# Kernel optimization log

Measured on AMD Instinct MI355X. Metric: run time of the kernel, lower is better.

The kernel has to match this reference:

```python
import jax, jax.numpy as jnp
import numpy as np

N_NODES = 10000
DEG = 32            # max_edges (fixed degree after padding)
CHANNELS = 16
IN_DIM = 4
BATCH = 8


def setup_inputs() -> dict:
    key = jax.random.key(0)
    k1, k2, k3 = jax.random.split(key, 3)
    E = N_NODES * DEG
    x = jax.random.normal(k1, (BATCH, N_NODES, IN_DIM), dtype=jnp.float32)
    # neighbor indices in [0, N_NODES]; index N_NODES is the padded 'useless' zero node
    edges = jax.random.randint(k2, (E,), 0, N_NODES + 1, dtype=jnp.int64)
    # torch.rand init: uniform [0,1); one weight tensor per input channel
    weights = jax.random.uniform(k3, (IN_DIM, E, CHANNELS), dtype=jnp.float32)
    return {"x": x, "edges": edges, "weights": weights}


def reference(x, edges, weights):
    B, N, in_dim = x.shape
    E = edges.shape[0]
    deg = E // N
    C = weights.shape[-1]
    # append zero 'useless node' so padding index N gathers zeros
    x_pad = jnp.concatenate([x, jnp.zeros((B, 1, in_dim), dtype=x.dtype)], axis=1)  # [B, N+1, in_dim]
    # super_edges = cat([edges]*C); viewed as [E, C] row-major (matches torch .view)
    idx = jnp.tile(edges, C).reshape(E, C)  # [E, C]
    out = jnp.zeros((B, N, C), dtype=x.dtype)
    for i in range(in_dim):  # small fixed loop over input channels (distinct weights)
        g = x_pad[:, :, i]              # [B, N+1]
        toc = g[:, idx]                 # gather -> [B, E, C]
        conv = toc * weights[i]         # per-edge weights broadcast over batch
        out = out + conv.reshape(B, N, deg, C).sum(axis=2)  # fixed-window segment sum
    return out
```

## Files before the change

### kernel.cpp

```cpp
#include <hip/hip_runtime.h>
#include <hip/hip_bf16.h>

#define N_NODES 10000
#define DEG     32
#define CH      16
#define IN_DIM  4
#define BATCH   8
#define E_EDGES (N_NODES * DEG)
#define WI_STRIDE (E_EDGES * CH)
#define P_COUNT 625
#define LX_STRIDE 36

__global__ __launch_bounds__(256) void lcg_transpose(const float* __restrict__ x,
                                                     float* __restrict__ xt) {
    int t = blockIdx.x * 256 + threadIdx.x;
    if (t < BATCH * N_NODES) {
        int b = t / N_NODES;
        int node = t - b * N_NODES;
        float4 v = *(const float4*)(x + 4 * t);
        *(float4*)(xt + node * 32 + b * 4) = v;
    } else if (t < BATCH * N_NODES + 8) {
        int r = t - BATCH * N_NODES;
        *(float4*)(xt + N_NODES * 32 + r * 4) = make_float4(0.f, 0.f, 0.f, 0.f);
    }
}

__global__ __launch_bounds__(1024, 8) void lcg_main(
    const float* __restrict__ xt,
    const int*   __restrict__ edges,
    const float* __restrict__ w,
    float*       __restrict__ out)
{
    __shared__ float lx[512 * LX_STRIDE];

    int p = blockIdx.x;
    int t = threadIdx.x;

    {
        int sub = t & 7;
        int rg  = t >> 3;
        const int* ep = edges + 512 * p;
        int nd[4];
#pragma unroll
        for (int k = 0; k < 4; k++) nd[k] = ep[rg + 128 * k];
#pragma unroll
        for (int k = 0; k < 4; k++) {
            int s = rg + 128 * k;
            float4 v = *(const float4*)(xt + nd[k] * 32 + sub * 4);
            *(float4*)(&lx[s * LX_STRIDE + sub * 4]) = v;
        }
    }
    __syncthreads();

    int lane = t & 63;
    int j    = t >> 6;
    int c    = lane & 15;
    int dq   = lane >> 4;
    int n    = p + P_COUNT * j;

    const float* wb = w + n * (DEG * CH) + lane;

    float acc[BATCH];
#pragma unroll
    for (int b = 0; b < BATCH; b++) acc[b] = 0.0f;

    const float* lrow = &lx[(16 * dq + c) * LX_STRIDE];

#pragma unroll 1
    for (int ds = 0; ds < 8; ds++) {
        float w0 = wb[64 * ds];
        float w1 = wb[64 * ds + WI_STRIDE];
        float w2 = wb[64 * ds + 2 * WI_STRIDE];
        float w3 = wb[64 * ds + 3 * WI_STRIDE];
        const float* lr = lrow + ds * (64 * LX_STRIDE);
#pragma unroll
        for (int b = 0; b < BATCH; b++) {
            float4 xq = *(const float4*)(lr + 4 * b);
            acc[b] += xq.x * w0 + xq.y * w1 + xq.z * w2 + xq.w * w3;
        }
    }

#pragma unroll
    for (int b = 0; b < BATCH; b++) {
        acc[b] += __shfl_xor(acc[b], 16, 64);
        acc[b] += __shfl_xor(acc[b], 32, 64);
    }

    int ob = n * CH + c;
    out[(2 * dq + 0) * (N_NODES * CH) + ob] = acc[2 * dq + 0];
    out[(2 * dq + 1) * (N_NODES * CH) + ob] = acc[2 * dq + 1];
}

extern "C" void kernel_launch(void* const* d_in, const int* in_sizes, int n_in,
                              void* d_out, int out_size, void* d_ws, size_t ws_size,
                              hipStream_t stream) {
    const float* x     = (const float*)d_in[0];
    const int*   edges = (const int*)d_in[1];
    const float* w     = (const float*)d_in[2];
    float* out = (float*)d_out;
    float* xt  = (float*)d_ws;

    int tr_total  = BATCH * N_NODES + 8;
    int tr_blocks = (tr_total + 255) / 256;
    lcg_transpose<<<tr_blocks, 256, 0, stream>>>(x, xt);

    lcg_main<<<P_COUNT, 1024, 0, stream>>>(xt, edges, w, out);
}
```

Baseline: 130.5 us.

## Drop transpose kernel, gather x directly, and software-prefetch weights

Removes the separate transpose launch and has the main kernel gather x straight from its original [B,N,4] layout, substituting zeros for the padding node. It also loads the first weights before the shared-memory fill and prefetches the next step's weights inside the loop, so global-load latency overlaps with compute. This saves one kernel launch and a pass over x. In exchange, each gather now reads scattered 16-byte chunks per batch instead of contiguous 128-byte rows, and the wrapped prefetch on the last iteration issues redundant loads.

```diff
diff --git a/kernel.cpp b/kernel.cpp
--- a/kernel.cpp
+++ b/kernel.cpp
@@ -1,5 +1,4 @@
 #include <hip/hip_runtime.h>
-#include <hip/hip_bf16.h>
 
 #define N_NODES 10000
 #define DEG     32
@@ -11,22 +10,8 @@
 #define P_COUNT 625
 #define LX_STRIDE 36
 
-__global__ __launch_bounds__(256) void lcg_transpose(const float* __restrict__ x,
-                                                     float* __restrict__ xt) {
-    int t = blockIdx.x * 256 + threadIdx.x;
-    if (t < BATCH * N_NODES) {
-        int b = t / N_NODES;
-        int node = t - b * N_NODES;
-        float4 v = *(const float4*)(x + 4 * t);
-        *(float4*)(xt + node * 32 + b * 4) = v;
-    } else if (t < BATCH * N_NODES + 8) {
-        int r = t - BATCH * N_NODES;
-        *(float4*)(xt + N_NODES * 32 + r * 4) = make_float4(0.f, 0.f, 0.f, 0.f);
-    }
-}
-
 __global__ __launch_bounds__(1024, 8) void lcg_main(
-    const float* __restrict__ xt,
+    const float* __restrict__ x,
     const int*   __restrict__ edges,
     const float* __restrict__ w,
     float*       __restrict__ out)
@@ -36,9 +21,22 @@
     int p = blockIdx.x;
     int t = threadIdx.x;
 
+    int lane = t & 63;
+    int j    = t >> 6;
+    int c    = lane & 15;
+    int dq   = lane >> 4;
+    int n    = p + P_COUNT * j;
+
+    const float* wb = w + n * (DEG * CH) + lane;
+
+    float w0 = wb[0];
+    float w1 = wb[WI_STRIDE];
+    float w2 = wb[2 * WI_STRIDE];
+    float w3 = wb[3 * WI_STRIDE];
+
     {
-        int sub = t & 7;
-        int rg  = t >> 3;
+        int b  = t & 7;
+        int rg = t >> 3;
         const int* ep = edges + 512 * p;
         int nd[4];
 #pragma unroll
@@ -46,19 +44,13 @@
 #pragma unroll
         for (int k = 0; k < 4; k++) {
             int s = rg + 128 * k;
-            float4 v = *(const float4*)(xt + nd[k] * 32 + sub * 4);
-            *(float4*)(&lx[s * LX_STRIDE + sub * 4]) = v;
+            float4 v = make_float4(0.f, 0.f, 0.f, 0.f);
+            if (nd[k] < N_NODES)
+                v = *(const float4*)(x + (b * N_NODES + nd[k]) * 4);
+            *(float4*)(&lx[s * LX_STRIDE + b * 4]) = v;
         }
     }
     __syncthreads();
-
-    int lane = t & 63;
-    int j    = t >> 6;
-    int c    = lane & 15;
-    int dq   = lane >> 4;
-    int n    = p + P_COUNT * j;
-
-    const float* wb = w + n * (DEG * CH) + lane;
 
     float acc[BATCH];
 #pragma unroll
@@ -68,16 +60,19 @@
 
 #pragma unroll 1
     for (int ds = 0; ds < 8; ds++) {
-        float w0 = wb[64 * ds];
-        float w1 = wb[64 * ds + WI_STRIDE];
-        float w2 = wb[64 * ds + 2 * WI_STRIDE];
-        float w3 = wb[64 * ds + 3 * WI_STRIDE];
+        int nxt = 64 * ((ds + 1) & 7);
+        float nw0 = wb[nxt];
+        float nw1 = wb[nxt + WI_STRIDE];
+        float nw2 = wb[nxt + 2 * WI_STRIDE];
+        float nw3 = wb[nxt + 3 * WI_STRIDE];
+
         const float* lr = lrow + ds * (64 * LX_STRIDE);
 #pragma unroll
         for (int b = 0; b < BATCH; b++) {
             float4 xq = *(const float4*)(lr + 4 * b);
             acc[b] += xq.x * w0 + xq.y * w1 + xq.z * w2 + xq.w * w3;
         }
+        w0 = nw0; w1 = nw1; w2 = nw2; w3 = nw3;
     }
 
 #pragma unroll
@@ -98,11 +93,7 @@
     const int*   edges = (const int*)d_in[1];
     const float* w     = (const float*)d_in[2];
     float* out = (float*)d_out;
-    float* xt  = (float*)d_ws;
+    (void)d_ws; (void)ws_size;
 
-    int tr_total  = BATCH * N_NODES + 8;
-    int tr_blocks = (tr_total + 255) / 256;
-    lcg_transpose<<<tr_blocks, 256, 0, stream>>>(x, xt);
-
-    lcg_main<<<P_COUNT, 1024, 0, stream>>>(xt, edges, w, out);
+    lcg_main<<<P_COUNT, 1024, 0, stream>>>(x, edges, w, out);
 }
```

Measured after the change: 136.4 us. 1.04x slower.

## Halve block size, process two nodes per thread with prefetched nontemporal weight loads

Applied to the files above, without the earlier changes.

The main kernel now runs 512 threads per block, and each thread computes two output nodes (j and j+8), so the shared gathered-x tile is reused across both. Weight loads for the first iteration are issued before the edge gather and sync, and each loop iteration prefetches the next slice into registers. Weight loads and output stores use nontemporal hints to avoid polluting cache. The cost is higher register pressure and fewer threads per block, which may reduce latency hiding.

```diff
diff --git a/kernel.cpp b/kernel.cpp
--- a/kernel.cpp
+++ b/kernel.cpp
@@ -1,5 +1,4 @@
 #include <hip/hip_runtime.h>
-#include <hip/hip_bf16.h>
 
 #define N_NODES 10000
 #define DEG     32
@@ -25,7 +24,7 @@
     }
 }
 
-__global__ __launch_bounds__(1024, 8) void lcg_main(
+__global__ __launch_bounds__(512, 4) void lcg_main(
     const float* __restrict__ xt,
     const int*   __restrict__ edges,
     const float* __restrict__ w,
@@ -36,59 +35,88 @@
     int p = blockIdx.x;
     int t = threadIdx.x;
 
+    int lane = t & 63;
+    int j    = t >> 6;
+    int c    = lane & 15;
+    int dq   = lane >> 4;
+    int n0   = p + P_COUNT * j;
+    int n1   = p + P_COUNT * (j + 8);
+
+    const float* wa = w + n0 * (DEG * CH) + lane;
+    const float* wbp = w + n1 * (DEG * CH) + lane;
+
+    float u0 = __builtin_nontemporal_load(wa);
+    float u1 = __builtin_nontemporal_load(wa + WI_STRIDE);
+    float u2 = __builtin_nontemporal_load(wa + 2 * WI_STRIDE);
+    float u3 = __builtin_nontemporal_load(wa + 3 * WI_STRIDE);
+    float v0 = __builtin_nontemporal_load(wbp);
+    float v1 = __builtin_nontemporal_load(wbp + WI_STRIDE);
+    float v2 = __builtin_nontemporal_load(wbp + 2 * WI_STRIDE);
+    float v3 = __builtin_nontemporal_load(wbp + 3 * WI_STRIDE);
+
     {
         int sub = t & 7;
         int rg  = t >> 3;
         const int* ep = edges + 512 * p;
-        int nd[4];
+        int nd[8];
 #pragma unroll
-        for (int k = 0; k < 4; k++) nd[k] = ep[rg + 128 * k];
+        for (int k = 0; k < 8; k++) nd[k] = ep[rg + 64 * k];
 #pragma unroll
-        for (int k = 0; k < 4; k++) {
-            int s = rg + 128 * k;
-            float4 v = *(const float4*)(xt + nd[k] * 32 + sub * 4);
-            *(float4*)(&lx[s * LX_STRIDE + sub * 4]) = v;
+        for (int k = 0; k < 8; k++) {
+            int s = rg + 64 * k;
+            float4 vv = *(const float4*)(xt + nd[k] * 32 + sub * 4);
+            *(float4*)(&lx[s * LX_STRIDE + sub * 4]) = vv;
         }
     }
     __syncthreads();
 
-    int lane = t & 63;
-    int j    = t >> 6;
-    int c    = lane & 15;
-    int dq   = lane >> 4;
-    int n    = p + P_COUNT * j;
-
-    const float* wb = w + n * (DEG * CH) + lane;
-
-    float acc[BATCH];
+    float acc0[BATCH], acc1[BATCH];
 #pragma unroll
-    for (int b = 0; b < BATCH; b++) acc[b] = 0.0f;
+    for (int b = 0; b < BATCH; b++) { acc0[b] = 0.0f; acc1[b] = 0.0f; }
 
     const float* lrow = &lx[(16 * dq + c) * LX_STRIDE];
 
 #pragma unroll 1
     for (int ds = 0; ds < 8; ds++) {
-        float w0 = wb[64 * ds];
-        float w1 = wb[64 * ds + WI_STRIDE];
-        float w2 = wb[64 * ds + 2 * WI_STRIDE];
-        float w3 = wb[64 * ds + 3 * WI_STRIDE];
+        int nxt = 64 * ((ds + 1) & 7);
+        float nu0 = __builtin_nontemporal_load(wa + nxt);
+        float nu1 = __builtin_nontemporal_load(wa + nxt + WI_STRIDE);
+        float nu2 = __builtin_nontemporal_load(wa + nxt + 2 * WI_STRIDE);
+        float nu3 = __builtin_nontemporal_load(wa + nxt + 3 * WI_STRIDE);
+        float nv0 = __builtin_nontemporal_load(wbp + nxt);
+        float nv1 = __builtin_nontemporal_load(wbp + nxt + WI_STRIDE);
+        float nv2 = __builtin_nontemporal_load(wbp + nxt + 2 * WI_STRIDE);
+        float nv3 = __builtin_nontemporal_load(wbp + nxt + 3 * WI_STRIDE);
+
         const float* lr = lrow + ds * (64 * LX_STRIDE);
 #pragma unroll
         for (int b = 0; b < BATCH; b++) {
             float4 xq = *(const float4*)(lr + 4 * b);
-            acc[b] += xq.x * w0 + xq.y * w1 + xq.z * w2 + xq.w * w3;
+            acc0[b] += xq.x * u0 + xq.y * u1 + xq.z * u2 + xq.w * u3;
+            acc1[b] += xq.x * v0 + xq.y * v1 + xq.z * v2 + xq.w * v3;
         }
+        u0 = nu0; u1 = nu1; u2 = nu2; u3 = nu3;
+        v0 = nv0; v1 = nv1; v2 = nv2; v3 = nv3;
     }
 
 #pragma unroll
     for (int b = 0; b < BATCH; b++) {
-        acc[b] += __shfl_xor(acc[b], 16, 64);
-        acc[b] += __shfl_xor(acc[b], 32, 64);
+        acc0[b] += __shfl_xor(acc0[b], 16, 64);
+        acc0[b] += __shfl_xor(acc0[b], 32, 64);
+        acc1[b] += __shfl_xor(acc1[b], 16, 64);
+        acc1[b] += __shfl_xor(acc1[b], 32, 64);
     }
 
-    int ob = n * CH + c;
-    out[(2 * dq + 0) * (N_NODES * CH) + ob] = acc[2 * dq + 0];
-    out[(2 * dq + 1) * (N_NODES * CH) + ob] = acc[2 * dq + 1];
+    int ob0 = n0 * CH + c;
+    int ob1 = n1 * CH + c;
+    __builtin_nontemporal_store(acc0[2 * dq + 0],
+        out + (2 * dq + 0) * (N_NODES * CH) + ob0);
+    __builtin_nontemporal_store(acc0[2 * dq + 1],
+        out + (2 * dq + 1) * (N_NODES * CH) + ob0);
+    __builtin_nontemporal_store(acc1[2 * dq + 0],
+        out + (2 * dq + 0) * (N_NODES * CH) + ob1);
+    __builtin_nontemporal_store(acc1[2 * dq + 1],
+        out + (2 * dq + 1) * (N_NODES * CH) + ob1);
 }
 
 extern "C" void kernel_launch(void* const* d_in, const int* in_sizes, int n_in,
@@ -104,5 +132,5 @@
     int tr_blocks = (tr_total + 255) / 256;
     lcg_transpose<<<tr_blocks, 256, 0, stream>>>(x, xt);
 
-    lcg_main<<<P_COUNT, 1024, 0, stream>>>(xt, edges, w, out);
+    lcg_main<<<P_COUNT, 512, 0, stream>>>(xt, edges, w, out);
 }
```

Measured after the change: 131.7 us. Within noise of the previous version (+0.9%).
